# Kernel optimization log

Hardware: AMD Instinct MI355X
Metric: run time of the kernel (lower is better)

The kernel has to match this reference:

```python
import jax, jax.numpy as jnp
import numpy as np

H = 20  # num heads; d_head = 1280 // 20 = 64


def setup_inputs() -> dict:
    key = jax.random.key(0)
    ks = jax.random.split(key, 7)
    B, S, C = 1, 2304, 1280
    hidden_states = jax.random.normal(ks[0], (B, S, C), dtype=jnp.float32)
    # structured boolean sparsity mask (True = keep); force diagonal True so no row is fully masked
    mask = jax.random.randint(ks[1], (S, S), 0, 2) > 0
    mask = mask | jnp.eye(S, dtype=bool)
    w_scale = 0.02  # keep logits in a sane range
    Wq = jax.random.normal(ks[2], (C, C), dtype=jnp.float32) * w_scale
    Wk = jax.random.normal(ks[3], (C, C), dtype=jnp.float32) * w_scale
    Wv = jax.random.normal(ks[4], (C, C), dtype=jnp.float32) * w_scale
    Wo = jax.random.normal(ks[5], (C, C), dtype=jnp.float32) * w_scale
    bo = jnp.zeros((C,), dtype=jnp.float32)
    return {"hidden_states": hidden_states, "mask": mask, "Wq": Wq, "Wk": Wk, "Wv": Wv, "Wo": Wo, "bo": bo}


def reference(hidden_states, mask, Wq, Wk, Wv, Wo, bo):
    B, S, C = hidden_states.shape
    d = C // H
    scale = 1.0 / jnp.sqrt(jnp.float32(d))
    # additive mask: masked_fill(mask == False, -inf)
    add_mask = jnp.where(mask, jnp.float32(0.0), -jnp.inf)  # [S, S]
    # projections (bias-free to_q/to_k/to_v as in diffusers)
    q = hidden_states @ Wq  # [B, S, C]
    k = hidden_states @ Wk
    v = hidden_states @ Wv
    # head_to_batch_dim: [B, S, C] -> [B, H, S, d]
    q = q.reshape(B, S, H, d).transpose(0, 2, 1, 3)
    k = k.reshape(B, S, H, d).transpose(0, 2, 1, 3)
    v = v.reshape(B, S, H, d).transpose(0, 2, 1, 3)
    # get_attention_scores: baddbmm(mask, q, k^T, alpha=scale, beta=1) then softmax
    scores = jnp.einsum("bhqd,bhkd->bhqk", q, k) * scale + add_mask
    probs = jax.nn.softmax(scores, axis=-1)  # [B, H, S, S]
    out = jnp.einsum("bhqk,bhkd->bhqd", probs, v)  # [B, H, S, d]
    # batch_to_head_dim: [B, H, S, d] -> [B, S, C]
    out = out.transpose(0, 2, 1, 3).reshape(B, S, C)
    # to_out[0] Linear + to_out[1] Dropout(eval = identity)
    out = out @ Wo + bo
    return out
```

## Files before the change

kernel.cpp:

```cpp
#include <hip/hip_runtime.h>
#include <stdint.h>

typedef __attribute__((ext_vector_type(8))) short short8;
typedef __attribute__((ext_vector_type(4))) float f32x4;
typedef unsigned short u16;
typedef unsigned int u32;

#define SEQ  2304
#define CDIM 1280
#define NH   20
#define DH   64
#define MW   72
#define SCL  0.18033688011112043f

__device__ __forceinline__ u16 f2bf(float x){
  u32 u = __builtin_bit_cast(u32, x);
  u += 0x7fffu + ((u >> 16) & 1u);
  return (u16)(u >> 16);
}

__device__ __forceinline__ void gload16(const void* g, void* l){
  auto gp = (const u32 __attribute__((address_space(1)))*)(uintptr_t)g;
  auto lp = (u32 __attribute__((address_space(3)))*)(uintptr_t)l;
  __builtin_amdgcn_global_load_lds(gp, lp, 16, 0, 0);
}

__global__ __launch_bounds__(256) void k_convert(const float* __restrict__ x, u16* __restrict__ y){
  int i = (blockIdx.x * 256 + threadIdx.x) * 4;
  float4 v = *(const float4*)(x + i);
  ushort4 o;
  o.x = f2bf(v.x); o.y = f2bf(v.y); o.z = f2bf(v.z); o.w = f2bf(v.w);
  *(ushort4*)(y + i) = o;
}

__global__ __launch_bounds__(256) void k_wt(const float* __restrict__ w0, const float* __restrict__ w1,
                                            const float* __restrict__ w2, const float* __restrict__ w3,
                                            u16* __restrict__ o0, u16* __restrict__ o1,
                                            u16* __restrict__ o2, u16* __restrict__ o3){
  const float* w = blockIdx.z==0 ? w0 : blockIdx.z==1 ? w1 : blockIdx.z==2 ? w2 : w3;
  u16* o        = blockIdx.z==0 ? o0 : blockIdx.z==1 ? o1 : blockIdx.z==2 ? o2 : o3;
  __shared__ u16 t[64][65];
  int bx = blockIdx.x*64, by = blockIdx.y*64, tid = threadIdx.x;
  #pragma unroll
  for (int i = 0; i < 16; i++){
    int idx = tid + i*256; int r = idx>>6, c = idx&63;
    t[r][c] = f2bf(w[(size_t)(by+r)*CDIM + bx + c]);
  }
  __syncthreads();
  #pragma unroll
  for (int i = 0; i < 16; i++){
    int idx = tid + i*256; int r = idx>>6, c = idx&63;
    o[(size_t)(bx+r)*CDIM + by + c] = t[c][r];
  }
}

__global__ __launch_bounds__(256) void k_vt(const u16* __restrict__ v, u16* __restrict__ vt){
  __shared__ u16 t[64][65];
  int bx = blockIdx.x*64, by = blockIdx.y*64, tid = threadIdx.x;
  #pragma unroll
  for (int i = 0; i < 16; i++){
    int idx = tid + i*256; int r = idx>>6, c = idx&63;
    t[r][c] = v[(size_t)(by+r)*CDIM + bx + c];
  }
  __syncthreads();
  #pragma unroll
  for (int i = 0; i < 16; i++){
    int idx = tid + i*256; int r = idx>>6, c = idx&63;
    vt[(size_t)(bx+r)*SEQ + by + c] = t[c][r];
  }
}

__global__ __launch_bounds__(256) void k_mask(const int* __restrict__ m, u32* __restrict__ mb){
  long long f = (long long)blockIdx.x * 256 + threadIdx.x;
  unsigned long long bal = __ballot(m[f] != 0);
  int lane = threadIdx.x & 63;
  if ((lane & 31) == 0) mb[f >> 5] = (u32)(bal >> (lane & 32));
}

template<int EPI>
__global__ __launch_bounds__(256) void k_gemm(const u16* __restrict__ A,
    const u16* __restrict__ B0, const u16* __restrict__ B1, const u16* __restrict__ B2,
    u16* __restrict__ O0, u16* __restrict__ O1, u16* __restrict__ O2,
    float* __restrict__ OF, const float* __restrict__ bias){
  const u16* B = blockIdx.z==0 ? B0 : blockIdx.z==1 ? B1 : B2;
  u16* O       = blockIdx.z==0 ? O0 : blockIdx.z==1 ? O1 : O2;
  __shared__ __align__(16) u16 Al[128*32];
  __shared__ __align__(16) u16 Bl[128*32];
  int tid = threadIdx.x, w = tid>>6, l = tid&63, c16 = l&15, g = l>>4;
  int wr = w>>1, wc = w&1;
  int m0 = blockIdx.y*128, n0 = blockIdx.x*128;
  f32x4 acc[4][4] = {};
  for (int kt = 0; kt < CDIM/32; ++kt){
    #pragma unroll
    for (int i = 0; i < 2; i++){
      int c = i*256 + w*64 + l;
      int r = c>>2, gr = c&3, sg = gr ^ ((r>>1)&3);
      gload16(A + (size_t)(m0+r)*CDIM + kt*32 + sg*8, &Al[(i*256 + w*64)*8]);
    }
    #pragma unroll
    for (int i = 0; i < 2; i++){
      int c = i*256 + w*64 + l;
      int r = c>>2, gr = c&3, sg = gr ^ ((r>>1)&3);
      gload16(B + (size_t)(n0+r)*CDIM + kt*32 + sg*8, &Bl[(i*256 + w*64)*8]);
    }
    __syncthreads();
    short8 af[4], bf[4];
    #pragma unroll
    for (int m = 0; m < 4; m++){
      int r = wr*64 + m*16 + c16; int sg = g ^ ((r>>1)&3);
      af[m] = *(const short8*)&Al[r*32 + sg*8];
    }
    #pragma unroll
    for (int n = 0; n < 4; n++){
      int r = wc*64 + n*16 + c16; int sg = g ^ ((r>>1)&3);
      bf[n] = *(const short8*)&Bl[r*32 + sg*8];
    }
    #pragma unroll
    for (int m = 0; m < 4; m++)
      #pragma unroll
      for (int n = 0; n < 4; n++)
        acc[m][n] = __builtin_amdgcn_mfma_f32_16x16x32_bf16(af[m], bf[n], acc[m][n], 0, 0, 0);
    __syncthreads();
  }
  #pragma unroll
  for (int m = 0; m < 4; m++)
    #pragma unroll
    for (int n = 0; n < 4; n++)
      #pragma unroll
      for (int r = 0; r < 4; r++){
        int row = m0 + wr*64 + m*16 + g*4 + r;
        int col = n0 + wc*64 + n*16 + c16;
        float v = acc[m][n][r];
        if constexpr (EPI == 0) O[(size_t)row*CDIM + col] = f2bf(v);
        else                    OF[(size_t)row*CDIM + col] = v + bias[col];
      }
}

__global__ __launch_bounds__(256) void k_attn(const u16* __restrict__ Q, const u16* __restrict__ K,
    const u16* __restrict__ Vt, const u32* __restrict__ mb, u16* __restrict__ O){
  __shared__ __align__(16) u16 Kl[128*64];
  __shared__ __align__(16) u16 Vl[64*128];
  __shared__ __align__(16) u16 Pl[4][16*128];
  __shared__ u32 Ml[256];
  int tid = threadIdx.x, w = tid>>6, l = tid&63, c16 = l&15, g = l>>4;
  int q0 = blockIdx.x*64, h = blockIdx.y;
  short8 qf[2];
  #pragma unroll
  for (int kf = 0; kf < 2; kf++)
    qf[kf] = *(const short8*)&Q[(size_t)(q0 + w*16 + c16)*CDIM + h*DH + kf*32 + g*8];
  f32x4 acc[4] = {};
  float mr[4] = {-__builtin_inff(), -__builtin_inff(), -__builtin_inff(), -__builtin_inff()};
  float lr[4] = {0.f, 0.f, 0.f, 0.f};
  const f32x4 zz = {0.f, 0.f, 0.f, 0.f};
  for (int kt = 0; kt < SEQ/128; ++kt){
    #pragma unroll
    for (int i = 0; i < 4; i++){
      int c = i*256 + w*64 + l;
      int r = c>>3, gr = c&7, sg = gr ^ (r&7);
      gload16(K + (size_t)(kt*128 + r)*CDIM + h*DH + sg*8, &Kl[(i*256 + w*64)*8]);
    }
    #pragma unroll
    for (int i = 0; i < 4; i++){
      int c = i*256 + w*64 + l;
      int r = c>>4, gr = c&15, sg = gr ^ (r&7);
      gload16(Vt + (size_t)(h*DH + r)*SEQ + kt*128 + sg*8, &Vl[(i*256 + w*64)*8]);
    }
    Ml[tid] = mb[(size_t)(q0 + (tid>>2))*MW + kt*4 + (tid&3)];
    __syncthreads();
    f32x4 s[8];
    #pragma unroll
    for (int fj = 0; fj < 8; fj++){
      s[fj] = zz;
      #pragma unroll
      for (int kf = 0; kf < 2; kf++){
        int rk = fj*16 + c16;
        int sg = (kf*4 + g) ^ (rk&7);
        short8 kb = *(const short8*)&Kl[rk*64 + sg*8];
        s[fj] = __builtin_amdgcn_mfma_f32_16x16x32_bf16(qf[kf], kb, s[fj], 0, 0, 0);
      }
    }
    u32 mwv[4][4];
    #pragma unroll
    for (int r = 0; r < 4; r++)
      #pragma unroll
      for (int wd = 0; wd < 4; wd++)
        mwv[r][wd] = Ml[(w*16 + g*4 + r)*4 + wd];
    #pragma unroll
    for (int fj = 0; fj < 8; fj++){
      int sh = ((fj&1) << 4) + c16;
      #pragma unroll
      for (int r = 0; r < 4; r++)
        s[fj][r] = ((mwv[r][fj>>1] >> sh) & 1u) ? s[fj][r]*SCL : -1e30f;
    }
    #pragma unroll
    for (int r = 0; r < 4; r++){
      float vm = s[0][r];
      #pragma unroll
      for (int fj = 1; fj < 8; fj++) vm = fmaxf(vm, s[fj][r]);
      vm = fmaxf(vm, __shfl_xor(vm, 1));
      vm = fmaxf(vm, __shfl_xor(vm, 2));
      vm = fmaxf(vm, __shfl_xor(vm, 4));
      vm = fmaxf(vm, __shfl_xor(vm, 8));
      float mn = fmaxf(mr[r], vm);
      float al = __builtin_exp2f(mr[r] - mn);
      mr[r] = mn;
      float sum = 0.f;
      #pragma unroll
      for (int fj = 0; fj < 8; fj++){ float p = __builtin_exp2f(s[fj][r] - mn); s[fj][r] = p; sum += p; }
      sum += __shfl_xor(sum, 1); sum += __shfl_xor(sum, 2);
      sum += __shfl_xor(sum, 4); sum += __shfl_xor(sum, 8);
      lr[r] = lr[r]*al + sum;
      #pragma unroll
      for (int n = 0; n < 4; n++) acc[n][r] *= al;
    }
    #pragma unroll
    for (int fj = 0; fj < 8; fj++){
      int colhi = fj*2 + (c16>>3);
      int cl = l & 7;
      #pragma unroll
      for (int r = 0; r < 4; r++){
        int pr = g*4 + r;
        Pl[w][pr*128 + ((colhi ^ (pr&7)) << 3) + cl] = f2bf(s[fj][r]);
      }
    }
    asm volatile("s_waitcnt lgkmcnt(0)" ::: "memory");
    short8 pa[4];
    #pragma unroll
    for (int kf = 0; kf < 4; kf++){
      int sg = (kf*4 + g) ^ (c16&7);
      pa[kf] = *(const short8*)&Pl[w][c16*128 + sg*8];
    }
    #pragma unroll
    for (int fj = 0; fj < 4; fj++)
      #pragma unroll
      for (int kf = 0; kf < 4; kf++){
        int rv = fj*16 + c16;
        int sg = (kf*4 + g) ^ (rv&7);
        short8 vb = *(const short8*)&Vl[rv*128 + sg*8];
        acc[fj] = __builtin_amdgcn_mfma_f32_16x16x32_bf16(pa[kf], vb, acc[fj], 0, 0, 0);
      }
    __syncthreads();
  }
  #pragma unroll
  for (int fj = 0; fj < 4; fj++)
    #pragma unroll
    for (int r = 0; r < 4; r++){
      int row = q0 + w*16 + g*4 + r;
      int col = h*DH + fj*16 + c16;
      O[(size_t)row*CDIM + col] = f2bf(acc[fj][r] / lr[r]);
    }
}

extern "C" void kernel_launch(void* const* d_in, const int* in_sizes, int n_in,
                              void* d_out, int out_size, void* d_ws, size_t ws_size,
                              hipStream_t stream){
  const float* X  = (const float*)d_in[0];
  const int*   Mk = (const int*)  d_in[1];
  const float* Wq = (const float*)d_in[2];
  const float* Wk = (const float*)d_in[3];
  const float* Wv = (const float*)d_in[4];
  const float* Wo = (const float*)d_in[5];
  const float* bo = (const float*)d_in[6];
  float* out = (float*)d_out;
  char* ws = (char*)d_ws;
  const size_t SZ_XB = (size_t)SEQ*CDIM*2;
  const size_t SZ_WT = (size_t)CDIM*CDIM*2;
  u16* Xb  = (u16*)(ws);
  u16* WqT = (u16*)(ws + SZ_XB);
  u16* WkT = (u16*)(ws + SZ_XB + 1*SZ_WT);
  u16* WvT = (u16*)(ws + SZ_XB + 2*SZ_WT);
  u16* WoT = (u16*)(ws + SZ_XB + 3*SZ_WT);
  u16* Qb  = (u16*)(ws + 1*SZ_XB + 4*SZ_WT);
  u16* Kb  = (u16*)(ws + 2*SZ_XB + 4*SZ_WT);
  u16* Vb  = (u16*)(ws + 3*SZ_XB + 4*SZ_WT);
  u16* Vt  = (u16*)(ws + 4*SZ_XB + 4*SZ_WT);
  u16* Ab  = (u16*)(ws + 5*SZ_XB + 4*SZ_WT);
  u32* mbp = (u32*)(ws + 6*SZ_XB + 4*SZ_WT);

  k_convert<<<2880, 256, 0, stream>>>(X, Xb);
  k_wt<<<dim3(20,20,4), 256, 0, stream>>>(Wq, Wk, Wv, Wo, WqT, WkT, WvT, WoT);
  k_mask<<<20736, 256, 0, stream>>>(Mk, mbp);
  k_gemm<0><<<dim3(10,18,3), 256, 0, stream>>>(Xb, WqT, WkT, WvT, Qb, Kb, Vb, nullptr, nullptr);
  k_vt<<<dim3(20,36), 256, 0, stream>>>(Vb, Vt);
  k_attn<<<dim3(36,20), 256, 0, stream>>>(Qb, Kb, Vt, mbp, Ab);
  k_gemm<1><<<dim3(10,18,1), 256, 0, stream>>>(Ab, WoT, WoT, WoT, nullptr, nullptr, nullptr, out, bo);
}
```

Measured before the change: 294.6 us.

## Compute transposed scores to keep P in registers, skipping LDS round-trip

The QK^T MFMA now has its operands swapped, so each lane holds scores for one query row across several keys. P can then be packed directly into the A operand with v_cvt_pk_bf16_f32, which removes the per-warp LDS staging of P. To match this register layout, V^T columns are written in a permuted key order, and the softmax scale is folded into the Q projection epilogue. The mask words are read straight from global memory per row instead of through shared memory, and the division is replaced by a reciprocal. This adds a permuted layout that must stay consistent between the V transpose and the PV MFMA, and it sets an occupancy hint of 4 blocks.

```diff
diff --git a/kernel.cpp b/kernel.cpp
--- a/kernel.cpp
+++ b/kernel.cpp
@@ -3,6 +3,7 @@
 
 typedef __attribute__((ext_vector_type(8))) short short8;
 typedef __attribute__((ext_vector_type(4))) float f32x4;
+typedef __attribute__((ext_vector_type(4))) unsigned int u32x4;
 typedef unsigned short u16;
 typedef unsigned int u32;
 
@@ -17,6 +18,12 @@
   u32 u = __builtin_bit_cast(u32, x);
   u += 0x7fffu + ((u >> 16) & 1u);
   return (u16)(u >> 16);
+}
+
+__device__ __forceinline__ u32 cvtpk(float lo, float hi){
+  u32 r;
+  asm("v_cvt_pk_bf16_f32 %0, %1, %2" : "=v"(r) : "v"(lo), "v"(hi));
+  return r;
 }
 
 __device__ __forceinline__ void gload16(const void* g, void* l){
@@ -66,7 +73,10 @@
   #pragma unroll
   for (int i = 0; i < 16; i++){
     int idx = tid + i*256; int r = idx>>6, c = idx&63;
-    vt[(size_t)(bx+r)*SEQ + by + c] = t[c][r];
+    int s = by + c;
+    int x = s & 127;
+    int nx = ((x>>5)<<5) | (((x>>2)&3)<<3) | (((x>>4)&1)<<2) | (x&3);
+    vt[(size_t)(bx+r)*SEQ + (s & ~127) + nx] = t[c][r];
   }
 }
 
@@ -84,6 +94,7 @@
     float* __restrict__ OF, const float* __restrict__ bias){
   const u16* B = blockIdx.z==0 ? B0 : blockIdx.z==1 ? B1 : B2;
   u16* O       = blockIdx.z==0 ? O0 : blockIdx.z==1 ? O1 : O2;
+  const float qs = (EPI==0 && blockIdx.z==0) ? SCL : 1.0f;
   __shared__ __align__(16) u16 Al[128*32];
   __shared__ __align__(16) u16 Bl[128*32];
   int tid = threadIdx.x, w = tid>>6, l = tid&63, c16 = l&15, g = l>>4;
@@ -131,26 +142,26 @@
         int row = m0 + wr*64 + m*16 + g*4 + r;
         int col = n0 + wc*64 + n*16 + c16;
         float v = acc[m][n][r];
-        if constexpr (EPI == 0) O[(size_t)row*CDIM + col] = f2bf(v);
+        if constexpr (EPI == 0) O[(size_t)row*CDIM + col] = f2bf(v * qs);
         else                    OF[(size_t)row*CDIM + col] = v + bias[col];
       }
 }
 
-__global__ __launch_bounds__(256) void k_attn(const u16* __restrict__ Q, const u16* __restrict__ K,
+__global__ __launch_bounds__(256, 4) void k_attn(const u16* __restrict__ Q, const u16* __restrict__ K,
     const u16* __restrict__ Vt, const u32* __restrict__ mb, u16* __restrict__ O){
   __shared__ __align__(16) u16 Kl[128*64];
   __shared__ __align__(16) u16 Vl[64*128];
-  __shared__ __align__(16) u16 Pl[4][16*128];
-  __shared__ u32 Ml[256];
   int tid = threadIdx.x, w = tid>>6, l = tid&63, c16 = l&15, g = l>>4;
+  int g4 = g*4;
   int q0 = blockIdx.x*64, h = blockIdx.y;
   short8 qf[2];
   #pragma unroll
   for (int kf = 0; kf < 2; kf++)
     qf[kf] = *(const short8*)&Q[(size_t)(q0 + w*16 + c16)*CDIM + h*DH + kf*32 + g*8];
+  const u32* mrow = mb + (size_t)(q0 + w*16 + c16)*MW;
   f32x4 acc[4] = {};
-  float mr[4] = {-__builtin_inff(), -__builtin_inff(), -__builtin_inff(), -__builtin_inff()};
-  float lr[4] = {0.f, 0.f, 0.f, 0.f};
+  float mr = -__builtin_inff();
+  float lr = 0.f;
   const f32x4 zz = {0.f, 0.f, 0.f, 0.f};
   for (int kt = 0; kt < SEQ/128; ++kt){
     #pragma unroll
@@ -165,7 +176,7 @@
       int r = c>>4, gr = c&15, sg = gr ^ (r&7);
       gload16(Vt + (size_t)(h*DH + r)*SEQ + kt*128 + sg*8, &Vl[(i*256 + w*64)*8]);
     }
-    Ml[tid] = mb[(size_t)(q0 + (tid>>2))*MW + kt*4 + (tid&3)];
+    u32x4 mw4 = *(const u32x4*)(mrow + kt*4);
     __syncthreads();
     f32x4 s[8];
     #pragma unroll
@@ -176,59 +187,56 @@
         int rk = fj*16 + c16;
         int sg = (kf*4 + g) ^ (rk&7);
         short8 kb = *(const short8*)&Kl[rk*64 + sg*8];
-        s[fj] = __builtin_amdgcn_mfma_f32_16x16x32_bf16(qf[kf], kb, s[fj], 0, 0, 0);
+        s[fj] = __builtin_amdgcn_mfma_f32_16x16x32_bf16(kb, qf[kf], s[fj], 0, 0, 0);
       }
     }
-    u32 mwv[4][4];
-    #pragma unroll
-    for (int r = 0; r < 4; r++)
-      #pragma unroll
-      for (int wd = 0; wd < 4; wd++)
-        mwv[r][wd] = Ml[(w*16 + g*4 + r)*4 + wd];
     #pragma unroll
     for (int fj = 0; fj < 8; fj++){
-      int sh = ((fj&1) << 4) + c16;
+      u32 mw = mw4[fj>>1] >> (((fj&1)<<4) + g4);
       #pragma unroll
       for (int r = 0; r < 4; r++)
-        s[fj][r] = ((mwv[r][fj>>1] >> sh) & 1u) ? s[fj][r]*SCL : -1e30f;
-    }
-    #pragma unroll
-    for (int r = 0; r < 4; r++){
-      float vm = s[0][r];
-      #pragma unroll
-      for (int fj = 1; fj < 8; fj++) vm = fmaxf(vm, s[fj][r]);
-      vm = fmaxf(vm, __shfl_xor(vm, 1));
-      vm = fmaxf(vm, __shfl_xor(vm, 2));
-      vm = fmaxf(vm, __shfl_xor(vm, 4));
-      vm = fmaxf(vm, __shfl_xor(vm, 8));
-      float mn = fmaxf(mr[r], vm);
-      float al = __builtin_exp2f(mr[r] - mn);
-      mr[r] = mn;
-      float sum = 0.f;
-      #pragma unroll
-      for (int fj = 0; fj < 8; fj++){ float p = __builtin_exp2f(s[fj][r] - mn); s[fj][r] = p; sum += p; }
-      sum += __shfl_xor(sum, 1); sum += __shfl_xor(sum, 2);
-      sum += __shfl_xor(sum, 4); sum += __shfl_xor(sum, 8);
-      lr[r] = lr[r]*al + sum;
-      #pragma unroll
-      for (int n = 0; n < 4; n++) acc[n][r] *= al;
-    }
+        s[fj][r] = (mw & (1u<<r)) ? s[fj][r] : -1e30f;
+    }
+    float t0, t1;
+    float vmf[8];
+    #pragma unroll
+    for (int fj = 0; fj < 8; fj++)
+      vmf[fj] = fmaxf(fmaxf(s[fj][0], s[fj][1]), fmaxf(s[fj][2], s[fj][3]));
+    t0 = fmaxf(fmaxf(vmf[0], vmf[1]), fmaxf(vmf[2], vmf[3]));
+    t1 = fmaxf(fmaxf(vmf[4], vmf[5]), fmaxf(vmf[6], vmf[7]));
+    float vm = fmaxf(t0, t1);
+    vm = fmaxf(vm, __shfl_xor(vm, 16));
+    vm = fmaxf(vm, __shfl_xor(vm, 32));
+    float mn = fmaxf(mr, vm);
+    float al = __builtin_exp2f(mr - mn);
+    mr = mn;
+    float al_bc[4];
+    #pragma unroll
+    for (int r = 0; r < 4; r++) al_bc[r] = __shfl(al, g4 + r);
+    #pragma unroll
+    for (int fj = 0; fj < 4; fj++)
+      #pragma unroll
+      for (int r = 0; r < 4; r++) acc[fj][r] *= al_bc[r];
+    float s0 = 0.f, s1 = 0.f, s2 = 0.f, s3 = 0.f;
     #pragma unroll
     for (int fj = 0; fj < 8; fj++){
-      int colhi = fj*2 + (c16>>3);
-      int cl = l & 7;
-      #pragma unroll
-      for (int r = 0; r < 4; r++){
-        int pr = g*4 + r;
-        Pl[w][pr*128 + ((colhi ^ (pr&7)) << 3) + cl] = f2bf(s[fj][r]);
-      }
-    }
-    asm volatile("s_waitcnt lgkmcnt(0)" ::: "memory");
+      float p0 = __builtin_exp2f(s[fj][0] - mn);
+      float p1 = __builtin_exp2f(s[fj][1] - mn);
+      float p2 = __builtin_exp2f(s[fj][2] - mn);
+      float p3 = __builtin_exp2f(s[fj][3] - mn);
+      s[fj][0] = p0; s[fj][1] = p1; s[fj][2] = p2; s[fj][3] = p3;
+      s0 += p0; s1 += p1; s2 += p2; s3 += p3;
+    }
+    lr = lr*al + ((s0 + s1) + (s2 + s3));
     short8 pa[4];
     #pragma unroll
     for (int kf = 0; kf < 4; kf++){
-      int sg = (kf*4 + g) ^ (c16&7);
-      pa[kf] = *(const short8*)&Pl[w][c16*128 + sg*8];
+      u32x4 pw;
+      pw[0] = cvtpk(s[2*kf  ][0], s[2*kf  ][1]);
+      pw[1] = cvtpk(s[2*kf  ][2], s[2*kf  ][3]);
+      pw[2] = cvtpk(s[2*kf+1][0], s[2*kf+1][1]);
+      pw[3] = cvtpk(s[2*kf+1][2], s[2*kf+1][3]);
+      pa[kf] = __builtin_bit_cast(short8, pw);
     }
     #pragma unroll
     for (int fj = 0; fj < 4; fj++)
@@ -241,13 +249,18 @@
       }
     __syncthreads();
   }
+  lr += __shfl_xor(lr, 16);
+  lr += __shfl_xor(lr, 32);
+  float inv[4];
+  #pragma unroll
+  for (int r = 0; r < 4; r++) inv[r] = __builtin_amdgcn_rcpf(__shfl(lr, g4 + r));
   #pragma unroll
   for (int fj = 0; fj < 4; fj++)
     #pragma unroll
     for (int r = 0; r < 4; r++){
-      int row = q0 + w*16 + g*4 + r;
+      int row = q0 + w*16 + g4 + r;
       int col = h*DH + fj*16 + c16;
-      O[(size_t)row*CDIM + col] = f2bf(acc[fj][r] / lr[r]);
+      O[(size_t)row*CDIM + col] = f2bf(acc[fj][r] * inv[r]);
     }
 }
 
```

New measurement: 245.4 us. 16.7% less time.
